# Performance work log

Hardware: AMD Instinct MI355X
Metric: run time of the kernel (lower is better)

Reference implementation:

```python
import jax, jax.numpy as jnp
import numpy as np

# Clos factorization for in=out=4096, middle_switch_multiplier=4:
BIN, B1, B2, B3, BOUT = 64, 64, 256, 64, 64
B, C, D = 2, 4096, 4096


def setup_inputs() -> dict:
    key = jax.random.key(0)
    ks = jax.random.split(key, 7)
    k = 1.0 / np.sqrt(D)
    x = jax.random.normal(ks[0], (B, C, D), dtype=jnp.float32)
    # kaiming_uniform(a=sqrt(5)) on [bin,b1,b2]-like tensors ~ uniform(-bound, bound)
    w1 = jax.random.uniform(ks[1], (BIN, B1, B2), jnp.float32, -k, k)
    w2 = jax.random.uniform(ks[2], (B1, B2, B3), jnp.float32, -k, k)
    w3 = jax.random.uniform(ks[3], (B2, B3, BOUT), jnp.float32, -k, k)
    bias1 = jax.random.uniform(ks[4], (B1,), jnp.float32, -k, k)
    bias2 = jax.random.uniform(ks[5], (B2,), jnp.float32, -k, k)
    bias3 = jax.random.uniform(ks[6], (B3,), jnp.float32, -k, k)
    return {"x": x, "w1": w1, "w2": w2, "w3": w3,
            "bias1": bias1, "bias2": bias2, "bias3": bias3}


def reference(x, w1, w2, w3, bias1, bias2, bias3):
    b, c, _ = x.shape
    h = x.reshape(b, c, BIN, B1)                      # [b,c,n=bin,r=b1]
    h = jnp.einsum('bcnr,nrm->bcmr', h, w1) + bias1   # [b,c,b2,b1] + bias over b1
    h = jnp.einsum('bcmr,rmn->bcnm', h, w2) + bias2   # [b,c,b3,b2] + bias over b2
    h = jnp.einsum('bcnm,mro->bcor', h, w3) + bias3   # [b,c,bout,b3] + bias over b3
    return h.reshape(b, c, -1)                        # [b,c,out_features]
```

## Files before the change

### kernel.cpp

```cpp
#include <hip/hip_runtime.h>
#include <stdint.h>
#include <stddef.h>

typedef __bf16 bf16_t;
typedef __bf16 bf16x8 __attribute__((ext_vector_type(8)));
typedef __bf16 bf16x4 __attribute__((ext_vector_type(4)));
typedef float f32x4 __attribute__((ext_vector_type(4)));

#define VMW(n) asm volatile("s_waitcnt vmcnt(" #n ")" ::: "memory")
#define CFENCE asm volatile("" ::: "memory")
#define RAWBAR              \
  do {                      \
    __builtin_amdgcn_s_barrier(); \
    CFENCE;                 \
  } while (0)

__device__ __forceinline__ void gload_lds16(const void* g, void* l) {
  __builtin_amdgcn_global_load_lds(
      (const __attribute__((address_space(1))) uint32_t*)g,
      (__attribute__((address_space(3))) uint32_t*)l, 16, 0, 0);
}

__global__ __launch_bounds__(256) void w2s_k(const float* __restrict__ w2,
                                             float* __restrict__ w2s) {
  const int r = blockIdx.x, m = threadIdx.x;
  const float4* p = (const float4*)(w2 + ((size_t)(r * 256 + m)) * 64);
  float s = 0.f;
#pragma unroll
  for (int i = 0; i < 16; ++i) {
    float4 v = p[i];
    s += (v.x + v.y) + (v.z + v.w);
  }
  w2s[r * 256 + m] = s;
}

__global__ __launch_bounds__(256) void prep_k(
    const float* __restrict__ w1, const float* __restrict__ w3,
    const float* __restrict__ w2s, const float* __restrict__ bias1,
    const float* __restrict__ bias2, bf16_t* __restrict__ w1t,
    bf16_t* __restrict__ w3pt, float* __restrict__ c2) {
  __shared__ float lds[64][65];
  const int b = blockIdx.x;
  const int t = threadIdx.x;
  if (b == 512) {
    float s = 64.f * bias2[t];
#pragma unroll 8
    for (int r = 0; r < 64; ++r) s += bias1[r] * w2s[r * 256 + t];
    c2[t] = s;
    return;
  }
  if (b < 256) {
    const int k0 = (b >> 2) * 64;
    const int mt = (b & 3) * 64;
#pragma unroll
    for (int it = 0; it < 16; ++it) {
      int idx = t + it * 256;
      int kl = idx >> 6, ml = idx & 63;
      int k = k0 + kl;
      lds[kl][ml] = w1[(size_t)k * 256 + mt + ml] * w2s[(k & 63) * 256 + mt + ml];
    }
    __syncthreads();
#pragma unroll
    for (int it = 0; it < 16; ++it) {
      int idx = t + it * 256;
      int ml = idx >> 6, kl = idx & 63;
      w1t[(size_t)(mt + ml) * 4096 + k0 + kl] = (bf16_t)lds[kl][ml];
    }
    return;
  }
  const int b2 = b - 256;
  const int r = b2 & 63;
  const int mt = (b2 >> 6) * 64;
#pragma unroll
  for (int it = 0; it < 16; ++it) {
    int idx = t + it * 256;
    int ml = idx >> 6, o = idx & 63;
    lds[ml][o] = w3[(size_t)(mt + ml) * 4096 + r * 64 + o];
  }
  __syncthreads();
#pragma unroll
  for (int it = 0; it < 16; ++it) {
    int idx = t + it * 256;
    int o = idx >> 6, ml = idx & 63;
    w3pt[(size_t)(o * 64 + r) * 256 + mt + ml] = (bf16_t)lds[ml][o];
  }
}

__global__ __launch_bounds__(256, 4) void gemm1_k(
    const float* __restrict__ X, const bf16_t* __restrict__ W1T,
    const float* __restrict__ c2, bf16_t* __restrict__ S) {
  __shared__ __align__(16) bf16_t lA[2][64 * 64];
  __shared__ __align__(16) bf16_t lB[2][64 * 64];
  const int tid = threadIdx.x;
  const int lane = tid & 63;
  const int wv = tid >> 6;
  const int bid = (int)blockIdx.x;
  const int xcd = bid & 7;
  const int rest = bid >> 3;
  const int mtile = xcd * 16 + (rest >> 2);
  const int n0 = (rest & 3) * 64;
  const size_t m0 = (size_t)mtile * 64;
  const int wm = wv >> 1, wn = wv & 1;
  const int ar = tid >> 2;
  const int acg = tid & 3;

  f32x4 acc[2][2];
#pragma unroll
  for (int i = 0; i < 2; ++i)
#pragma unroll
    for (int j = 0; j < 2; ++j) acc[i][j] = (f32x4){0.f, 0.f, 0.f, 0.f};

  float4 aR[4];

  auto issueA = [&](int kt) {
#pragma unroll
    for (int j = 0; j < 4; ++j) {
      int f4 = acg + j * 4;
      aR[j] = *(const float4*)(X + (m0 + ar) * 4096 + (size_t)(kt * 64 + f4 * 4));
    }
  };
  auto writeA = [&](int buf) {
#pragma unroll
    for (int j = 0; j < 4; ++j) {
      int f4 = acg + j * 4;
      int off = ar * 128 + ((f4 * 8) ^ ((ar & 7) << 4));
      bf16x4 v;
      v[0] = (bf16_t)aR[j].x;
      v[1] = (bf16_t)aR[j].y;
      v[2] = (bf16_t)aR[j].z;
      v[3] = (bf16_t)aR[j].w;
      *(bf16x4*)((char*)(&lA[buf][0]) + off) = v;
    }
  };
  auto issueB = [&](int buf, int kt) {
#pragma unroll
    for (int i = 0; i < 2; ++i) {
      int row = wv * 16 + i * 8 + (lane >> 3);
      int srckb = ((lane & 7) * 16) ^ ((row & 7) << 4);
      const char* src = (const char*)W1T + (size_t)(n0 + row) * 8192 + (size_t)(kt * 128) + srckb;
      char* dst = (char*)(&lB[buf][0]) + (wv * 16 + i * 8) * 128;
      gload_lds16(src, dst);
    }
  };
  auto compute = [&](int buf) {
#pragma unroll
    for (int kk = 0; kk < 2; ++kk) {
      const int kb = kk * 64 + ((lane >> 4) * 16);
      bf16x8 af[2], bfr[2];
#pragma unroll
      for (int mf = 0; mf < 2; ++mf) {
        int row = wm * 32 + mf * 16 + (lane & 15);
        int off = row * 128 + (kb ^ ((row & 7) << 4));
        af[mf] = *(const bf16x8*)((const char*)(&lA[buf][0]) + off);
      }
#pragma unroll
      for (int nf = 0; nf < 2; ++nf) {
        int row = wn * 32 + nf * 16 + (lane & 15);
        int off = row * 128 + (kb ^ ((row & 7) << 4));
        bfr[nf] = *(const bf16x8*)((const char*)(&lB[buf][0]) + off);
      }
#pragma unroll
      for (int mf = 0; mf < 2; ++mf)
#pragma unroll
        for (int nf = 0; nf < 2; ++nf)
          acc[mf][nf] = __builtin_amdgcn_mfma_f32_16x16x32_bf16(af[mf], bfr[nf], acc[mf][nf], 0, 0, 0);
    }
  };

  issueA(0);
  issueB(0, 0);
  writeA(0);
  __syncthreads();

#pragma unroll 1
  for (int kt = 0; kt < 64; ++kt) {
    int cur = kt & 1;
    bool more = (kt + 1) < 64;
    if (more) {
      issueA(kt + 1);
      issueB(cur ^ 1, kt + 1);
    }
    compute(cur);
    if (more) writeA(cur ^ 1);
    __syncthreads();
  }

#pragma unroll
  for (int nf = 0; nf < 2; ++nf) {
    int col = n0 + wn * 32 + nf * 16 + (lane & 15);
    float cadd = c2[col];
#pragma unroll
    for (int mf = 0; mf < 2; ++mf) {
#pragma unroll
      for (int q = 0; q < 4; ++q) {
        int row = wm * 32 + mf * 16 + (lane >> 4) * 4 + q;
        S[(m0 + row) * 256 + (size_t)col] = (bf16_t)(acc[mf][nf][q] + cadd);
      }
    }
  }
}

__global__ __launch_bounds__(512, 2) void gemm2_k(
    const bf16_t* __restrict__ S, const bf16_t* __restrict__ W3pT,
    const float* __restrict__ bias3, float* __restrict__ OUT) {
  __shared__ __align__(16) bf16_t lA[2][128 * 64];
  __shared__ __align__(16) bf16_t lB[2][256 * 64];
  const int tid = threadIdx.x;
  const int lane = tid & 63;
  const int wv = tid >> 6;
  const int bid = (int)blockIdx.x;
  const int xcd = bid & 7;
  const int rest = bid >> 3;
  const int mt = xcd * 8 + (rest >> 4);
  const int nt = rest & 15;
  const size_t m0 = (size_t)mt * 128;
  const int n0 = nt * 256;
  const int wm = wv >> 2, wn = wv & 3;

  f32x4 acc[4][4];
#pragma unroll
  for (int i = 0; i < 4; ++i)
#pragma unroll
    for (int j = 0; j < 4; ++j) acc[i][j] = (f32x4){0.f, 0.f, 0.f, 0.f};

  auto stage = [&](int buf, int kt) {
#pragma unroll
    for (int i = 0; i < 2; ++i) {
      int row = wv * 16 + i * 8 + (lane >> 3);
      int srckb = ((lane & 7) * 16) ^ ((row & 7) << 4);
      const char* srcA = (const char*)S + (m0 + row) * 512 + (size_t)(kt * 128) + srckb;
      char* dstA = (char*)(&lA[buf][0]) + (wv * 16 + i * 8) * 128;
      gload_lds16(srcA, dstA);
    }
#pragma unroll
    for (int i = 0; i < 4; ++i) {
      int row = wv * 32 + i * 8 + (lane >> 3);
      int srckb = ((lane & 7) * 16) ^ ((row & 7) << 4);
      const char* srcB = (const char*)W3pT + (size_t)(n0 + row) * 512 + (size_t)(kt * 128) + srckb;
      char* dstB = (char*)(&lB[buf][0]) + (wv * 32 + i * 8) * 128;
      gload_lds16(srcB, dstB);
    }
  };
  auto compute = [&](int buf) {
#pragma unroll
    for (int kk = 0; kk < 2; ++kk) {
      const int kb = kk * 64 + ((lane >> 4) * 16);
      bf16x8 af[4], bfr[4];
#pragma unroll
      for (int mf = 0; mf < 4; ++mf) {
        int row = wm * 64 + mf * 16 + (lane & 15);
        int off = row * 128 + (kb ^ ((row & 7) << 4));
        af[mf] = *(const bf16x8*)((const char*)(&lA[buf][0]) + off);
      }
#pragma unroll
      for (int nf = 0; nf < 4; ++nf) {
        int row = wn * 64 + nf * 16 + (lane & 15);
        int off = row * 128 + (kb ^ ((row & 7) << 4));
        bfr[nf] = *(const bf16x8*)((const char*)(&lB[buf][0]) + off);
      }
#pragma unroll
      for (int mf = 0; mf < 4; ++mf)
#pragma unroll
        for (int nf = 0; nf < 4; ++nf)
          acc[mf][nf] = __builtin_amdgcn_mfma_f32_16x16x32_bf16(af[mf], bfr[nf], acc[mf][nf], 0, 0, 0);
    }
  };

  stage(0, 0);
  CFENCE;
  stage(1, 1);
  CFENCE;
  VMW(6);
  RAWBAR;
  compute(0);
  RAWBAR;
  stage(0, 2);
  CFENCE;
  VMW(6);
  RAWBAR;
  compute(1);
  RAWBAR;
  stage(1, 3);
  CFENCE;
  VMW(6);
  RAWBAR;
  compute(0);
  RAWBAR;
  VMW(0);
  RAWBAR;
  compute(1);

#pragma unroll
  for (int nf = 0; nf < 4; ++nf) {
    int jcol = wn * 64 + nf * 16 + (lane & 15);
    float b3 = bias3[jcol & 63];
    int j = n0 + jcol;
#pragma unroll
    for (int mf = 0; mf < 4; ++mf) {
#pragma unroll
      for (int q = 0; q < 4; ++q) {
        size_t row = m0 + (size_t)(wm * 64 + mf * 16 + (lane >> 4) * 4 + q);
        OUT[row * 4096 + j] = acc[mf][nf][q] + b3;
      }
    }
  }
}

extern "C" void kernel_launch(void* const* d_in, const int* in_sizes, int n_in,
                              void* d_out, int out_size, void* d_ws, size_t ws_size,
                              hipStream_t stream) {
  (void)in_sizes; (void)n_in; (void)out_size; (void)ws_size;
  const float* x  = (const float*)d_in[0];
  const float* w1 = (const float*)d_in[1];
  const float* w2 = (const float*)d_in[2];
  const float* w3 = (const float*)d_in[3];
  const float* b1 = (const float*)d_in[4];
  const float* b2 = (const float*)d_in[5];
  const float* b3 = (const float*)d_in[6];
  float* out = (float*)d_out;
  char* ws = (char*)d_ws;

  float*  w2s  = (float*)(ws + 0);
  float*  c2   = (float*)(ws + 65536);
  bf16_t* w1t  = (bf16_t*)(ws + 69632);
  bf16_t* w3pt = (bf16_t*)(ws + 69632 + 2097152);
  bf16_t* S    = (bf16_t*)(ws + 69632 + 2 * 2097152);

  w2s_k<<<64, 256, 0, stream>>>(w2, w2s);
  prep_k<<<513, 256, 0, stream>>>(w1, w3, w2s, b1, b2, w1t, w3pt, c2);
  gemm1_k<<<512, 256, 0, stream>>>(x, w1t, c2, S);
  gemm2_k<<<1024, 512, 0, stream>>>(S, w3pt, b3, out);
}
```

Measured before the change: 123.3 us.

## Split-K gemm1 with full-N tiles and separate bf16 partial-sum reduce kernel

```diff
diff --git a/kernel.cpp b/kernel.cpp
--- a/kernel.cpp
+++ b/kernel.cpp
@@ -86,11 +86,11 @@
   }
 }
 
-__global__ __launch_bounds__(256, 4) void gemm1_k(
+__global__ __launch_bounds__(256, 2) void gemm1_k(
     const float* __restrict__ X, const bf16_t* __restrict__ W1T,
-    const float* __restrict__ c2, bf16_t* __restrict__ S) {
+    bf16_t* __restrict__ S4) {
   __shared__ __align__(16) bf16_t lA[2][64 * 64];
-  __shared__ __align__(16) bf16_t lB[2][64 * 64];
+  __shared__ __align__(16) bf16_t lB[2][256 * 64];
   const int tid = threadIdx.x;
   const int lane = tid & 63;
   const int wv = tid >> 6;
@@ -98,17 +98,18 @@
   const int xcd = bid & 7;
   const int rest = bid >> 3;
   const int mtile = xcd * 16 + (rest >> 2);
-  const int n0 = (rest & 3) * 64;
+  const int ks = rest & 3;
   const size_t m0 = (size_t)mtile * 64;
+  const int kbase = ks * 1024;
   const int wm = wv >> 1, wn = wv & 1;
   const int ar = tid >> 2;
   const int acg = tid & 3;
 
-  f32x4 acc[2][2];
+  f32x4 acc[2][8];
 #pragma unroll
   for (int i = 0; i < 2; ++i)
 #pragma unroll
-    for (int j = 0; j < 2; ++j) acc[i][j] = (f32x4){0.f, 0.f, 0.f, 0.f};
+    for (int j = 0; j < 8; ++j) acc[i][j] = (f32x4){0.f, 0.f, 0.f, 0.f};
 
   float4 aR[4];
 
@@ -116,7 +117,7 @@
 #pragma unroll
     for (int j = 0; j < 4; ++j) {
       int f4 = acg + j * 4;
-      aR[j] = *(const float4*)(X + (m0 + ar) * 4096 + (size_t)(kt * 64 + f4 * 4));
+      aR[j] = *(const float4*)(X + (m0 + ar) * 4096 + (size_t)(kbase + kt * 64 + f4 * 4));
     }
   };
   auto writeA = [&](int buf) {
@@ -134,11 +135,11 @@
   };
   auto issueB = [&](int buf, int kt) {
 #pragma unroll
-    for (int i = 0; i < 2; ++i) {
-      int row = wv * 16 + i * 8 + (lane >> 3);
+    for (int i = 0; i < 8; ++i) {
+      int row = wv * 64 + i * 8 + (lane >> 3);
       int srckb = ((lane & 7) * 16) ^ ((row & 7) << 4);
-      const char* src = (const char*)W1T + (size_t)(n0 + row) * 8192 + (size_t)(kt * 128) + srckb;
-      char* dst = (char*)(&lB[buf][0]) + (wv * 16 + i * 8) * 128;
+      const char* src = (const char*)W1T + (size_t)row * 8192 + (size_t)(kbase + kt * 64) * 2 + srckb;
+      char* dst = (char*)(&lB[buf][0]) + (wv * 64 + i * 8) * 128;
       gload_lds16(src, dst);
     }
   };
@@ -146,7 +147,7 @@
 #pragma unroll
     for (int kk = 0; kk < 2; ++kk) {
       const int kb = kk * 64 + ((lane >> 4) * 16);
-      bf16x8 af[2], bfr[2];
+      bf16x8 af[2], bfr[8];
 #pragma unroll
       for (int mf = 0; mf < 2; ++mf) {
         int row = wm * 32 + mf * 16 + (lane & 15);
@@ -154,15 +155,15 @@
         af[mf] = *(const bf16x8*)((const char*)(&lA[buf][0]) + off);
       }
 #pragma unroll
-      for (int nf = 0; nf < 2; ++nf) {
-        int row = wn * 32 + nf * 16 + (lane & 15);
+      for (int nf = 0; nf < 8; ++nf) {
+        int row = wn * 128 + nf * 16 + (lane & 15);
         int off = row * 128 + (kb ^ ((row & 7) << 4));
         bfr[nf] = *(const bf16x8*)((const char*)(&lB[buf][0]) + off);
       }
 #pragma unroll
       for (int mf = 0; mf < 2; ++mf)
 #pragma unroll
-        for (int nf = 0; nf < 2; ++nf)
+        for (int nf = 0; nf < 8; ++nf)
           acc[mf][nf] = __builtin_amdgcn_mfma_f32_16x16x32_bf16(af[mf], bfr[nf], acc[mf][nf], 0, 0, 0);
     }
   };
@@ -173,9 +174,9 @@
   __syncthreads();
 
 #pragma unroll 1
-  for (int kt = 0; kt < 64; ++kt) {
+  for (int kt = 0; kt < 16; ++kt) {
     int cur = kt & 1;
-    bool more = (kt + 1) < 64;
+    bool more = (kt + 1) < 16;
     if (more) {
       issueA(kt + 1);
       issueB(cur ^ 1, kt + 1);
@@ -186,18 +187,42 @@
   }
 
 #pragma unroll
-  for (int nf = 0; nf < 2; ++nf) {
-    int col = n0 + wn * 32 + nf * 16 + (lane & 15);
-    float cadd = c2[col];
+  for (int nf = 0; nf < 8; ++nf) {
+    int col = wn * 128 + nf * 16 + (lane & 15);
 #pragma unroll
     for (int mf = 0; mf < 2; ++mf) {
 #pragma unroll
       for (int q = 0; q < 4; ++q) {
         int row = wm * 32 + mf * 16 + (lane >> 4) * 4 + q;
-        S[(m0 + row) * 256 + (size_t)col] = (bf16_t)(acc[mf][nf][q] + cadd);
-      }
-    }
-  }
+        S4[(m0 + row) * 1024 + (size_t)(ks * 256 + col)] = (bf16_t)acc[mf][nf][q];
+      }
+    }
+  }
+}
+
+__global__ __launch_bounds__(256) void reduce_k(
+    const bf16_t* __restrict__ S4, const float* __restrict__ c2,
+    bf16_t* __restrict__ S) {
+  const int bid = (int)blockIdx.x;
+  const int base = (bid & 7) * 1024 + (bid >> 3) * 8;
+  const int t = threadIdx.x;
+  const int row = base + (t >> 5);
+  const int c8 = (t & 31) << 3;
+  float s[8];
+  float4 ca = *(const float4*)(c2 + c8);
+  float4 cb = *(const float4*)(c2 + c8 + 4);
+  s[0] = ca.x; s[1] = ca.y; s[2] = ca.z; s[3] = ca.w;
+  s[4] = cb.x; s[5] = cb.y; s[6] = cb.z; s[7] = cb.w;
+#pragma unroll
+  for (int h = 0; h < 4; ++h) {
+    bf16x8 v = *(const bf16x8*)(S4 + (size_t)row * 1024 + h * 256 + c8);
+#pragma unroll
+    for (int j = 0; j < 8; ++j) s[j] += (float)v[j];
+  }
+  bf16x8 o;
+#pragma unroll
+  for (int j = 0; j < 8; ++j) o[j] = (bf16_t)s[j];
+  *(bf16x8*)(S + (size_t)row * 256 + c8) = o;
 }
 
 __global__ __launch_bounds__(512, 2) void gemm2_k(
@@ -324,10 +349,12 @@
   float*  c2   = (float*)(ws + 65536);
   bf16_t* w1t  = (bf16_t*)(ws + 69632);
   bf16_t* w3pt = (bf16_t*)(ws + 69632 + 2097152);
-  bf16_t* S    = (bf16_t*)(ws + 69632 + 2 * 2097152);
+  bf16_t* S4   = (bf16_t*)(ws + 69632 + 2 * 2097152);
+  bf16_t* S    = (bf16_t*)(ws + 69632 + 2 * 2097152 + 16777216);
 
   w2s_k<<<64, 256, 0, stream>>>(w2, w2s);
   prep_k<<<513, 256, 0, stream>>>(w1, w3, w2s, b1, b2, w1t, w3pt, c2);
-  gemm1_k<<<512, 256, 0, stream>>>(x, w1t, c2, S);
+  gemm1_k<<<512, 256, 0, stream>>>(x, w1t, S4);
+  reduce_k<<<1024, 256, 0, stream>>>(S4, c2, S);
   gemm2_k<<<1024, 512, 0, stream>>>(S, w3pt, b3, out);
 }
```

New measurement: 104.5 us. -15.3%, faster.
